# Optimization experiments

Measured on AMD Instinct MI355X. Metric: run time of the kernel, lower is better.

## Reference

```python
import jax, jax.numpy as jnp
import numpy as np

B, T, D, H = 2, 2048, 1024, 16
HD = D // H  # head dim = 64

def build_rope(t, half, base=10000.0):
    inv = 1.0 / (base ** (jnp.arange(0, half, dtype=jnp.float32) / half))
    ang = jnp.arange(t, dtype=jnp.float32)[:, None] * inv[None, :]  # (T, half)
    return jnp.stack([jnp.cos(ang), jnp.sin(ang)], axis=-1)  # (T, half, 2)

def setup_inputs() -> dict:
    key = jax.random.key(0)
    k1, k2, k3 = jax.random.split(key, 3)
    x = jax.random.normal(k1, (B, T, D), dtype=jnp.float32)
    W_attn = jax.random.normal(k2, (D, 3 * D), dtype=jnp.float32) * (1.0 / np.sqrt(D))
    W_proj = jax.random.normal(k3, (D, D), dtype=jnp.float32) * (1.0 / np.sqrt(D))
    rope = build_rope(T, HD // 2)
    mask = jnp.tril(jnp.ones((T, T), dtype=bool))[None, None]  # (1,1,T,T) causal
    return {"x": x, "rope": rope, "W_attn": W_attn, "W_proj": W_proj, "mask": mask}

def apply_rope(xq, rope):
    # xq: (B, T, H, HD); rope: (T, HD//2, 2)
    xs = xq.astype(jnp.float32).reshape(*xq.shape[:-1], -1, 2)        # (B,T,H,HD/2,2)
    rc = rope[:xq.shape[1]].reshape(1, xq.shape[1], 1, xs.shape[3], 2)  # (1,T,1,HD/2,2)
    out = jnp.stack([
        xs[..., 0] * rc[..., 0] - xs[..., 1] * rc[..., 1],
        xs[..., 1] * rc[..., 0] + xs[..., 0] * rc[..., 1],
    ], axis=-1)
    return out.reshape(xq.shape).astype(xq.dtype)

def reference(x, rope, W_attn, W_proj, mask):
    b, t, d = x.shape
    qkv = x @ W_attn                                   # (B,T,3D)
    q, k, v = jnp.split(qkv, 3, axis=2)
    q = apply_rope(q.reshape(b, t, H, HD), rope)
    k = apply_rope(k.reshape(b, t, H, HD), rope)
    v = v.reshape(b, t, H, HD)
    # (B,H,T,HD)
    q = q.transpose(0, 2, 1, 3)
    k = k.transpose(0, 2, 1, 3)
    v = v.transpose(0, 2, 1, 3)
    scale = 1.0 / np.sqrt(HD)
    scores = jnp.einsum('bhqd,bhkd->bhqk', q, k) * scale
    scores = jnp.where(mask, scores, jnp.finfo(scores.dtype).min)
    attn = jax.nn.softmax(scores, axis=-1)
    out = jnp.einsum('bhqk,bhkd->bhqd', attn, v)       # (B,H,T,HD)
    out = out.transpose(0, 2, 1, 3).reshape(b, t, d)
    return out @ W_proj
```

## Files before the change

kernel.cpp:

```cpp
#include <hip/hip_runtime.h>


typedef __bf16 bf16x8 __attribute__((ext_vector_type(8)));
typedef float f32x4 __attribute__((ext_vector_type(4)));

__device__ __forceinline__ float bf2f(unsigned short u) {
  unsigned int i = ((unsigned int)u) << 16;
  return __builtin_bit_cast(float, i);
}
__device__ __forceinline__ unsigned short f2bf(float f) {
  unsigned int i = __builtin_bit_cast(unsigned int, f);
  i += 0x7FFFu + ((i >> 16) & 1u);
  return (unsigned short)(i >> 16);
}
__device__ __forceinline__ unsigned int pack2(float a, float b) {
  return (unsigned int)f2bf(a) | ((unsigned int)f2bf(b) << 16);
}

__device__ __forceinline__ void gload_lds16(const unsigned short* g, unsigned short* l) {
  __builtin_amdgcn_global_load_lds(
      (const __attribute__((address_space(1))) void*)g,
      (__attribute__((address_space(3))) void*)l, 16, 0, 0);
}

__global__ __launch_bounds__(256) void convert_f32_bf16_kernel(
    const float* __restrict__ in, unsigned short* __restrict__ outp, int n8)
{
  int i = blockIdx.x * 256 + threadIdx.x;
  if (i >= n8) return;
  const float4 a0 = *reinterpret_cast<const float4*>(&in[(size_t)i * 8]);
  const float4 a1 = *reinterpret_cast<const float4*>(&in[(size_t)i * 8 + 4]);
  uint4 pk;
  pk.x = pack2(a0.x, a0.y);
  pk.y = pack2(a0.z, a0.w);
  pk.z = pack2(a1.x, a1.y);
  pk.w = pack2(a1.z, a1.w);
  *reinterpret_cast<uint4*>(&outp[(size_t)i * 8]) = pk;
}

__global__ __launch_bounds__(256) void convert_transpose_kernel(
    const float* __restrict__ W, unsigned short* __restrict__ WT, int R, int C)
{
  __shared__ unsigned short tileT[64][72];
  const int c0 = blockIdx.x * 64, r0 = blockIdx.y * 64;
  const int tid = threadIdx.x;
  const int rr = tid >> 4, cc = (tid & 15) * 4;
#pragma unroll
  for (int it = 0; it < 4; ++it) {
    int gr = r0 + rr + it * 16;
    float4 v = *reinterpret_cast<const float4*>(&W[(size_t)gr * C + c0 + cc]);
    tileT[cc + 0][rr + it * 16] = f2bf(v.x);
    tileT[cc + 1][rr + it * 16] = f2bf(v.y);
    tileT[cc + 2][rr + it * 16] = f2bf(v.z);
    tileT[cc + 3][rr + it * 16] = f2bf(v.w);
  }
  __syncthreads();
  const int wc = tid >> 2, wk = (tid & 3) * 16;
  uint4 o0 = *reinterpret_cast<const uint4*>(&tileT[wc][wk]);
  uint4 o1 = *reinterpret_cast<const uint4*>(&tileT[wc][wk + 8]);
  unsigned short* dst = &WT[(size_t)(c0 + wc) * R + r0 + wk];
  *reinterpret_cast<uint4*>(dst) = o0;
  *reinterpret_cast<uint4*>(dst + 8) = o1;
}

__global__ __launch_bounds__(256) void transpose_v_kernel(
    const unsigned short* __restrict__ Vb, unsigned short* __restrict__ VT)
{
  __shared__ unsigned short tl[64][72];
  const int bh = blockIdx.y;
  const int t0 = blockIdx.x * 64;
  const int tid = threadIdx.x;
  const unsigned short* src = Vb + (size_t)bh * 2048 * 64;
  unsigned short* dst = VT + (size_t)bh * 64 * 2048;
  int row = tid >> 3, c8 = (tid & 7) * 8;
#pragma unroll
  for (int it = 0; it < 2; ++it, row += 32) {
    uint4 v = *reinterpret_cast<const uint4*>(&src[(size_t)(t0 + row) * 64 + c8]);
    *reinterpret_cast<uint4*>(&tl[row][c8]) = v;
  }
  __syncthreads();
  const int d = tid >> 2, tc = (tid & 3) * 16;
  unsigned int o[8];
#pragma unroll
  for (int j = 0; j < 8; ++j) {
    unsigned int lo  = tl[tc + 2 * j][d];
    unsigned int hi2 = tl[tc + 2 * j + 1][d];
    o[j] = lo | (hi2 << 16);
  }
  unsigned short* dp = &dst[(size_t)d * 2048 + t0 + tc];
  *reinterpret_cast<uint4*>(dp)     = uint4{o[0], o[1], o[2], o[3]};
  *reinterpret_cast<uint4*>(dp + 8) = uint4{o[4], o[5], o[6], o[7]};
}

template<bool C_IS_F32>
__global__ __launch_bounds__(256) void gemm_bt_kernel(
    const unsigned short* __restrict__ A, const unsigned short* __restrict__ BT,
    void* __restrict__ Cp, int M, int N, int K)
{
  __shared__ alignas(16) unsigned short As[128 * 32];
  __shared__ alignas(16) unsigned short Bs[128 * 32];

  const int tid = threadIdx.x;
  const int m0 = blockIdx.y * 128, n0 = blockIdx.x * 128;
  const int w = tid >> 6, lane = tid & 63;
  const int wr = (w >> 1) * 64, wc = (w & 1) * 64;
  const int g = lane >> 4, r = lane & 15;

  f32x4 acc[4][4];
#pragma unroll
  for (int i = 0; i < 4; ++i)
#pragma unroll
    for (int j = 0; j < 4; ++j)
      acc[i][j] = f32x4{0.f, 0.f, 0.f, 0.f};

  const int srow = w * 32 + (lane >> 2);
  const int sk = (lane & 3) << 3;
  const size_t a_base = (size_t)(m0 + srow) * K + sk;
  const size_t b_base = (size_t)(n0 + srow) * K + sk;
  unsigned short* lA = &As[w * 1024 + lane * 8];
  unsigned short* lB = &Bs[w * 1024 + lane * 8];
  const size_t rstep = (size_t)16 * K;

  for (int k0 = 0; k0 < K; k0 += 32) {
    __syncthreads();
    gload_lds16(&A[a_base + k0], lA);
    gload_lds16(&A[a_base + k0 + rstep], lA + 512);
    gload_lds16(&BT[b_base + k0], lB);
    gload_lds16(&BT[b_base + k0 + rstep], lB + 512);
    __syncthreads();

    bf16x8 af[4], bff[4];
#pragma unroll
    for (int i = 0; i < 4; ++i)
      af[i] = __builtin_bit_cast(bf16x8,
          *reinterpret_cast<const uint4*>(&As[(wr + i * 16 + r) * 32 + g * 8]));
#pragma unroll
    for (int j = 0; j < 4; ++j)
      bff[j] = __builtin_bit_cast(bf16x8,
          *reinterpret_cast<const uint4*>(&Bs[(wc + j * 16 + r) * 32 + g * 8]));
#pragma unroll
    for (int i = 0; i < 4; ++i)
#pragma unroll
      for (int j = 0; j < 4; ++j)
        acc[i][j] = __builtin_amdgcn_mfma_f32_16x16x32_bf16(af[i], bff[j], acc[i][j], 0, 0, 0);
  }

#pragma unroll
  for (int i = 0; i < 4; ++i)
#pragma unroll
    for (int j = 0; j < 4; ++j)
#pragma unroll
      for (int reg = 0; reg < 4; ++reg) {
        int row = m0 + wr + i * 16 + g * 4 + reg;
        int col = n0 + wc + j * 16 + r;
        if constexpr (C_IS_F32)
          ((float*)Cp)[(size_t)row * N + col] = acc[i][j][reg];
        else
          ((unsigned short*)Cp)[(size_t)row * N + col] = f2bf(acc[i][j][reg]);
      }
}

__global__ __launch_bounds__(256) void rope_scatter_kernel(
    const unsigned short* __restrict__ qkv, const float* __restrict__ rope,
    unsigned short* __restrict__ Qb, unsigned short* __restrict__ Kb,
    unsigned short* __restrict__ Vb)
{
  int gid = blockIdx.x * 256 + threadIdx.x;
  int rowM = gid / 768;
  int c4 = (gid - rowM * 768) * 4;
  int b = rowM >> 11, t = rowM & 2047;
  int sec = c4 >> 10;
  int d = c4 & 1023;
  int h = d >> 6, hd = d & 63;

  uint2 vv = *reinterpret_cast<const uint2*>(&qkv[(size_t)rowM * 3072 + c4]);
  size_t dst = ((size_t)(b * 16 + h) * 2048 + t) * 64 + hd;

  if (sec == 2) {
    *reinterpret_cast<uint2*>(&Vb[dst]) = vv;
    return;
  }
  float x0 = bf2f((unsigned short)(vv.x & 0xffffu));
  float x1 = bf2f((unsigned short)(vv.x >> 16));
  float x2 = bf2f((unsigned short)(vv.y & 0xffffu));
  float x3 = bf2f((unsigned short)(vv.y >> 16));
  float4 rc = *reinterpret_cast<const float4*>(&rope[(size_t)t * 64 + hd]);
  float y0 = x0 * rc.x - x1 * rc.y;
  float y1 = x1 * rc.x + x0 * rc.y;
  float y2 = x2 * rc.z - x3 * rc.w;
  float y3 = x3 * rc.z + x2 * rc.w;
  uint2 outv;
  outv.x = pack2(y0, y1);
  outv.y = pack2(y2, y3);
  unsigned short* dstp = (sec == 0) ? Qb : Kb;
  *reinterpret_cast<uint2*>(&dstp[dst]) = outv;
}

__global__ __launch_bounds__(512, 4) void attn_mfma_kernel(
    const unsigned short* __restrict__ Q, const unsigned short* __restrict__ K,
    const unsigned short* __restrict__ VT, unsigned short* __restrict__ O)
{
  __shared__ unsigned short Ks[2][64 * 64];
  __shared__ unsigned short Vs[2][64 * 64];

  const int bx = blockIdx.x;
  const int idx = bx & 255, hi = bx >> 8;
  const int bh = hi * 16 + (idx >> 4);
  const int tp = idx & 15;
  const int tile = hi ? tp : 15 - tp;
  const int b = bh >> 4, h = bh & 15;
  const size_t base = (size_t)bh * 2048 * 64;
  const unsigned short* VTb = VT + (size_t)bh * 64 * 2048;

  const int tid = threadIdx.x, w = tid >> 6, lane = tid & 63;
  const int g = lane >> 4, r = lane & 15;
  const int q0 = tile * 128;
  const int wrow0 = q0 + w * 16;

  bf16x8 qf[2];
#pragma unroll
  for (int kk = 0; kk < 2; ++kk)
    qf[kk] = __builtin_bit_cast(bf16x8, *reinterpret_cast<const uint4*>(
        &Q[base + (size_t)(wrow0 + r) * 64 + kk * 32 + g * 8]));

  float m = -1e30f, l = 0.f;
  f32x4 ov[4];
#pragma unroll
  for (int df = 0; df < 4; ++df) ov[df] = f32x4{0.f, 0.f, 0.f, 0.f};

  const int srow = tid >> 3, sc8 = (tid & 7) * 8;
  const unsigned short* Kg = &K[base + (size_t)srow * 64 + sc8];
  const unsigned short* Vg = &VTb[(size_t)srow * 2048 + sc8];
  const int sb = srow * 128 + ((sc8 * 2) ^ ((srow & 7) << 4));

  const float cs = 0.125f * 1.44269504f;
  const int nkt = (q0 >> 6) + 2;

  const int srcA = ((g & 1) << 5) | r;
  const int srcB = srcA | 16;
  const bool hsel = (g >> 1) != 0;

  uint4 kreg = *reinterpret_cast<const uint4*>(Kg);
  uint4 vreg = *reinterpret_cast<const uint4*>(Vg);
  *reinterpret_cast<uint4*>((char*)Ks[0] + sb) = kreg;
  *reinterpret_cast<uint4*>((char*)Vs[0] + sb) = vreg;
  __syncthreads();

  for (int c = 0; c < nkt; ++c) {
    const int kb = c * 64;
    const int cur = c & 1;
    const bool pfn = (c + 1 < nkt);
    if (pfn) {
      kreg = *reinterpret_cast<const uint4*>(Kg + (size_t)(kb + 64) * 64);
      vreg = *reinterpret_cast<const uint4*>(Vg + kb + 64);
    }

    if (kb <= wrow0 + 15) {
      f32x4 s[4];
#pragma unroll
      for (int cf = 0; cf < 4; ++cf) s[cf] = f32x4{0.f, 0.f, 0.f, 0.f};
      __builtin_amdgcn_s_setprio(1);
#pragma unroll
      for (int kk = 0; kk < 2; ++kk) {
#pragma unroll
        for (int cf = 0; cf < 4; ++cf) {
          int row = cf * 16 + r;
          const char* p = (const char*)Ks[cur] + row * 128 + ((kk * 64 + g * 16) ^ ((r & 7) << 4));
          bf16x8 kf = __builtin_bit_cast(bf16x8, *reinterpret_cast<const uint4*>(p));
          s[cf] = __builtin_amdgcn_mfma_f32_16x16x32_bf16(kf, qf[kk], s[cf], 0, 0, 0);
        }
      }
      __builtin_amdgcn_s_setprio(0);

      if (kb + 63 > wrow0) {
#pragma unroll
        for (int cf = 0; cf < 4; ++cf) {
          int keyb = kb + cf * 16 + g * 4;
#pragma unroll
          for (int reg = 0; reg < 4; ++reg)
            if (keyb + reg > wrow0 + r) s[cf][reg] = -1e30f;
        }
      }

      float vmx = s[0][0];
#pragma unroll
      for (int cf = 0; cf < 4; ++cf)
#pragma unroll
        for (int reg = 0; reg < 4; ++reg)
          vmx = fmaxf(vmx, s[cf][reg]);
      vmx = fmaxf(vmx, __shfl_xor(vmx, 16));
      vmx = fmaxf(vmx, __shfl_xor(vmx, 32));
      float mo = m;
      float mn = fmaxf(mo, vmx);
      float al = __builtin_amdgcn_exp2f((mo - mn) * cs);
      m = mn;
      float ps = 0.f;
#pragma unroll
      for (int cf = 0; cf < 4; ++cf)
#pragma unroll
        for (int reg = 0; reg < 4; ++reg) {
          float p = __builtin_amdgcn_exp2f((s[cf][reg] - mn) * cs);
          s[cf][reg] = p;
          ps += p;
        }
      l = l * al + ps;
#pragma unroll
      for (int df = 0; df < 4; ++df) ov[df] *= al;

      unsigned int pk[4][2];
#pragma unroll
      for (int cf = 0; cf < 4; ++cf) {
        pk[cf][0] = pack2(s[cf][0], s[cf][1]);
        pk[cf][1] = pack2(s[cf][2], s[cf][3]);
      }

      __builtin_amdgcn_s_setprio(1);
#pragma unroll
      for (int kk = 0; kk < 2; ++kk) {
        unsigned int a0 = __shfl(pk[2 * kk][0], srcA), b0 = __shfl(pk[2 * kk + 1][0], srcA);
        unsigned int a1 = __shfl(pk[2 * kk][1], srcA), b1 = __shfl(pk[2 * kk + 1][1], srcA);
        unsigned int a2 = __shfl(pk[2 * kk][0], srcB), b2 = __shfl(pk[2 * kk + 1][0], srcB);
        unsigned int a3 = __shfl(pk[2 * kk][1], srcB), b3 = __shfl(pk[2 * kk + 1][1], srcB);
        uint4 pw{ hsel ? b0 : a0, hsel ? b1 : a1, hsel ? b2 : a2, hsel ? b3 : a3 };
        bf16x8 pf = __builtin_bit_cast(bf16x8, pw);
#pragma unroll
        for (int df = 0; df < 4; ++df) {
          int row = df * 16 + r;
          const char* p = (const char*)Vs[cur] + row * 128 + ((kk * 64 + g * 16) ^ ((r & 7) << 4));
          bf16x8 vf = __builtin_bit_cast(bf16x8, *reinterpret_cast<const uint4*>(p));
          ov[df] = __builtin_amdgcn_mfma_f32_16x16x32_bf16(vf, pf, ov[df], 0, 0, 0);
        }
      }
      __builtin_amdgcn_s_setprio(0);
    }

    if (pfn) {
      *reinterpret_cast<uint4*>((char*)Ks[cur ^ 1] + sb) = kreg;
      *reinterpret_cast<uint4*>((char*)Vs[cur ^ 1] + sb) = vreg;
    }
    __syncthreads();
  }

  float ls = l;
  ls += __shfl_xor(ls, 16);
  ls += __shfl_xor(ls, 32);
  float inv = 1.f / ls;
  size_t orow = (size_t)(b * 2048 + wrow0 + r) * 1024 + h * 64 + g * 4;
#pragma unroll
  for (int df = 0; df < 4; ++df) {
    uint2 o;
    o.x = pack2(ov[df][0] * inv, ov[df][1] * inv);
    o.y = pack2(ov[df][2] * inv, ov[df][3] * inv);
    *reinterpret_cast<uint2*>(&O[orow + df * 16]) = o;
  }
}

extern "C" void kernel_launch(void* const* d_in, const int* in_sizes, int n_in,
                              void* d_out, int out_size, void* d_ws, size_t ws_size,
                              hipStream_t stream)
{
  (void)in_sizes; (void)n_in; (void)out_size; (void)ws_size;
  const float* x    = (const float*)d_in[0];
  const float* rope = (const float*)d_in[1];
  const float* Wa   = (const float*)d_in[2];
  const float* Wp   = (const float*)d_in[3];

  unsigned short* ws  = (unsigned short*)d_ws;
  unsigned short* qkv = ws;
  unsigned short* Qb  = qkv + (size_t)4096 * 3072;
  unsigned short* Kb  = Qb + (size_t)32 * 2048 * 64;
  unsigned short* Vb  = Kb + (size_t)32 * 2048 * 64;
  unsigned short* WpT = Vb + (size_t)32 * 2048 * 64;
  unsigned short* xb  = Qb;
  unsigned short* WaT = Kb;
  unsigned short* O   = qkv;
  unsigned short* VT  = qkv + (size_t)4096 * 1024;
  float* out = (float*)d_out;

  convert_f32_bf16_kernel<<<2048, 256, 0, stream>>>(x, xb, 4096 * 1024 / 8);
  convert_transpose_kernel<<<dim3(48, 16), 256, 0, stream>>>(Wa, WaT, 1024, 3072);
  convert_transpose_kernel<<<dim3(16, 16), 256, 0, stream>>>(Wp, WpT, 1024, 1024);
  gemm_bt_kernel<false><<<dim3(3072 / 128, 4096 / 128), 256, 0, stream>>>(
      xb, WaT, qkv, 4096, 3072, 1024);
  rope_scatter_kernel<<<(4096 * 3072 / 4) / 256, 256, 0, stream>>>(qkv, rope, Qb, Kb, Vb);
  transpose_v_kernel<<<dim3(32, 32), 256, 0, stream>>>(Vb, VT);
  attn_mfma_kernel<<<512, 512, 0, stream>>>(Qb, Kb, VT, O);
  gemm_bt_kernel<true><<<dim3(1024 / 128, 4096 / 128), 256, 0, stream>>>(
      O, WpT, out, 4096, 1024, 1024);
}
```

Before: 225.7 us.

## Fuse prep kernels, stage bf16 GEMM epilogue via LDS, add lazy softmax rescale

Merges the three input-conversion kernels into one launch that dispatches by block index. The bf16 GEMM epilogue now packs results with a hardware convert instruction, stages them in a padded shared tile and writes them out as coalesced 16-byte stores, replacing scattered 2-byte stores. The attention kernel skips the running-max update and the output rescale when the new block max stays within a fixed threshold, and uses the packed bf16 convert for P and the output. The lazy rescale allows exp values up to 2^4 before renormalizing, which trades a little numerical headroom for fewer rescale operations.

```diff
diff --git a/kernel.cpp b/kernel.cpp
--- a/kernel.cpp
+++ b/kernel.cpp
@@ -16,6 +16,11 @@
 __device__ __forceinline__ unsigned int pack2(float a, float b) {
   return (unsigned int)f2bf(a) | ((unsigned int)f2bf(b) << 16);
 }
+__device__ __forceinline__ unsigned int cvtpk(float a, float b) {
+  unsigned int r;
+  asm("v_cvt_pk_bf16_f32 %0, %1, %2" : "=v"(r) : "v"(a), "v"(b));
+  return r;
+}
 
 __device__ __forceinline__ void gload_lds16(const unsigned short* g, unsigned short* l) {
   __builtin_amdgcn_global_load_lds(
@@ -23,27 +28,38 @@
       (__attribute__((address_space(3))) void*)l, 16, 0, 0);
 }
 
-__global__ __launch_bounds__(256) void convert_f32_bf16_kernel(
-    const float* __restrict__ in, unsigned short* __restrict__ outp, int n8)
-{
-  int i = blockIdx.x * 256 + threadIdx.x;
-  if (i >= n8) return;
-  const float4 a0 = *reinterpret_cast<const float4*>(&in[(size_t)i * 8]);
-  const float4 a1 = *reinterpret_cast<const float4*>(&in[(size_t)i * 8 + 4]);
-  uint4 pk;
-  pk.x = pack2(a0.x, a0.y);
-  pk.y = pack2(a0.z, a0.w);
-  pk.z = pack2(a1.x, a1.y);
-  pk.w = pack2(a1.z, a1.w);
-  *reinterpret_cast<uint4*>(&outp[(size_t)i * 8]) = pk;
-}
-
-__global__ __launch_bounds__(256) void convert_transpose_kernel(
-    const float* __restrict__ W, unsigned short* __restrict__ WT, int R, int C)
+__global__ __launch_bounds__(256) void prep_kernel(
+    const float* __restrict__ x, unsigned short* __restrict__ xb,
+    const float* __restrict__ Wa, unsigned short* __restrict__ WaT,
+    const float* __restrict__ Wp, unsigned short* __restrict__ WpT)
 {
   __shared__ unsigned short tileT[64][72];
-  const int c0 = blockIdx.x * 64, r0 = blockIdx.y * 64;
-  const int tid = threadIdx.x;
+  const int bid = blockIdx.x, tid = threadIdx.x;
+
+  if (bid < 2048) {
+    int i = bid * 256 + tid;
+    const float4 a0 = *reinterpret_cast<const float4*>(&x[(size_t)i * 8]);
+    const float4 a1 = *reinterpret_cast<const float4*>(&x[(size_t)i * 8 + 4]);
+    uint4 pk;
+    pk.x = pack2(a0.x, a0.y);
+    pk.y = pack2(a0.z, a0.w);
+    pk.z = pack2(a1.x, a1.y);
+    pk.w = pack2(a1.z, a1.w);
+    *reinterpret_cast<uint4*>(&xb[(size_t)i * 8]) = pk;
+    return;
+  }
+  const float* W;
+  unsigned short* WT;
+  int R, C, c0, r0;
+  if (bid < 2816) {
+    int tb = bid - 2048;
+    W = Wa; WT = WaT; R = 1024; C = 3072;
+    c0 = (tb % 48) * 64; r0 = (tb / 48) * 64;
+  } else {
+    int tb = bid - 2816;
+    W = Wp; WT = WpT; R = 1024; C = 1024;
+    c0 = (tb % 16) * 64; r0 = (tb / 16) * 64;
+  }
   const int rr = tid >> 4, cc = (tid & 15) * 4;
 #pragma unroll
   for (int it = 0; it < 4; ++it) {
@@ -97,8 +113,9 @@
     const unsigned short* __restrict__ A, const unsigned short* __restrict__ BT,
     void* __restrict__ Cp, int M, int N, int K)
 {
-  __shared__ alignas(16) unsigned short As[128 * 32];
-  __shared__ alignas(16) unsigned short Bs[128 * 32];
+  __shared__ alignas(16) unsigned short smem[16896];
+  unsigned short* As = smem;
+  unsigned short* Bs = smem + 4096;
 
   const int tid = threadIdx.x;
   const int m0 = blockIdx.y * 128, n0 = blockIdx.x * 128;
@@ -145,19 +162,43 @@
         acc[i][j] = __builtin_amdgcn_mfma_f32_16x16x32_bf16(af[i], bff[j], acc[i][j], 0, 0, 0);
   }
 
-#pragma unroll
-  for (int i = 0; i < 4; ++i)
-#pragma unroll
-    for (int j = 0; j < 4; ++j)
-#pragma unroll
-      for (int reg = 0; reg < 4; ++reg) {
-        int row = m0 + wr + i * 16 + g * 4 + reg;
-        int col = n0 + wc + j * 16 + r;
-        if constexpr (C_IS_F32)
+  if constexpr (!C_IS_F32) {
+    __syncthreads();
+    unsigned short* ct = smem;
+#pragma unroll
+    for (int i = 0; i < 4; ++i)
+#pragma unroll
+      for (int j = 0; j < 4; ++j) {
+        int row0 = wr + i * 16 + g * 4;
+        int col  = wc + j * 16 + r;
+        unsigned int w01 = cvtpk(acc[i][j][0], acc[i][j][1]);
+        unsigned int w23 = cvtpk(acc[i][j][2], acc[i][j][3]);
+        ct[(row0 + 0) * 132 + col] = (unsigned short)(w01 & 0xffffu);
+        ct[(row0 + 1) * 132 + col] = (unsigned short)(w01 >> 16);
+        ct[(row0 + 2) * 132 + col] = (unsigned short)(w23 & 0xffffu);
+        ct[(row0 + 3) * 132 + col] = (unsigned short)(w23 >> 16);
+      }
+    __syncthreads();
+    unsigned short* C = (unsigned short*)Cp;
+    const int prow = tid >> 4, pcol = (tid & 15) * 8;
+#pragma unroll
+    for (int p = 0; p < 8; ++p) {
+      int row = p * 16 + prow;
+      uint4 v = *reinterpret_cast<const uint4*>(&ct[row * 132 + pcol]);
+      *reinterpret_cast<uint4*>(&C[(size_t)(m0 + row) * N + n0 + pcol]) = v;
+    }
+  } else {
+#pragma unroll
+    for (int i = 0; i < 4; ++i)
+#pragma unroll
+      for (int j = 0; j < 4; ++j)
+#pragma unroll
+        for (int reg = 0; reg < 4; ++reg) {
+          int row = m0 + wr + i * 16 + g * 4 + reg;
+          int col = n0 + wc + j * 16 + r;
           ((float*)Cp)[(size_t)row * N + col] = acc[i][j][reg];
-        else
-          ((unsigned short*)Cp)[(size_t)row * N + col] = f2bf(acc[i][j][reg]);
-      }
+        }
+  }
 }
 
 __global__ __launch_bounds__(256) void rope_scatter_kernel(
@@ -291,9 +332,16 @@
       vmx = fmaxf(vmx, __shfl_xor(vmx, 16));
       vmx = fmaxf(vmx, __shfl_xor(vmx, 32));
       float mo = m;
-      float mn = fmaxf(mo, vmx);
-      float al = __builtin_amdgcn_exp2f((mo - mn) * cs);
-      m = mn;
+      float mn, al;
+      if (__all((vmx - mo) * cs <= 4.0f)) {
+        mn = mo; al = 1.0f;
+      } else {
+        mn = fmaxf(mo, vmx);
+        al = __builtin_amdgcn_exp2f((mo - mn) * cs);
+        m = mn;
+#pragma unroll
+        for (int df = 0; df < 4; ++df) ov[df] *= al;
+      }
       float ps = 0.f;
 #pragma unroll
       for (int cf = 0; cf < 4; ++cf)
@@ -304,14 +352,12 @@
           ps += p;
         }
       l = l * al + ps;
-#pragma unroll
-      for (int df = 0; df < 4; ++df) ov[df] *= al;
 
       unsigned int pk[4][2];
 #pragma unroll
       for (int cf = 0; cf < 4; ++cf) {
-        pk[cf][0] = pack2(s[cf][0], s[cf][1]);
-        pk[cf][1] = pack2(s[cf][2], s[cf][3]);
+        pk[cf][0] = cvtpk(s[cf][0], s[cf][1]);
+        pk[cf][1] = cvtpk(s[cf][2], s[cf][3]);
       }
 
       __builtin_amdgcn_s_setprio(1);
@@ -349,8 +395,8 @@
 #pragma unroll
   for (int df = 0; df < 4; ++df) {
     uint2 o;
-    o.x = pack2(ov[df][0] * inv, ov[df][1] * inv);
-    o.y = pack2(ov[df][2] * inv, ov[df][3] * inv);
+    o.x = cvtpk(ov[df][0] * inv, ov[df][1] * inv);
+    o.y = cvtpk(ov[df][2] * inv, ov[df][3] * inv);
     *reinterpret_cast<uint2*>(&O[orow + df * 16]) = o;
   }
 }
@@ -377,9 +423,7 @@
   unsigned short* VT  = qkv + (size_t)4096 * 1024;
   float* out = (float*)d_out;
 
-  convert_f32_bf16_kernel<<<2048, 256, 0, stream>>>(x, xb, 4096 * 1024 / 8);
-  convert_transpose_kernel<<<dim3(48, 16), 256, 0, stream>>>(Wa, WaT, 1024, 3072);
-  convert_transpose_kernel<<<dim3(16, 16), 256, 0, stream>>>(Wp, WpT, 1024, 1024);
+  prep_kernel<<<3072, 256, 0, stream>>>(x, xb, Wa, WaT, Wp, WpT);
   gemm_bt_kernel<false><<<dim3(3072 / 128, 4096 / 128), 256, 0, stream>>>(
       xb, WaT, qkv, 4096, 3072, 1024);
   rope_scatter_kernel<<<(4096 * 3072 / 4) / 256, 256, 0, stream>>>(qkv, rope, Qb, Kb, Vb);
```

New measurement: 222.6 us. No clear change (-1.4%).
